# Kernel optimization log

Hardware: AMD Instinct MI355X
Metric: run time of the kernel (lower is better)

The kernel has to match this reference:

```python
import jax, jax.numpy as jnp
import numpy as np

HIDDEN = 512
HEADS = 8
HEAD_DIM = HIDDEN // HEADS
N = 262144
G = 1024
LN_EPS = 1e-5
EPS = 1e-8


def setup_inputs() -> dict:
    key = jax.random.key(0)
    ks = jax.random.split(key, 4)
    x = jax.random.normal(ks[0], (N, HIDDEN), dtype=jnp.float32)
    batch = jnp.sort(jax.random.randint(ks[1], (N,), 0, G, dtype=jnp.int32))
    gamma = jnp.ones((HIDDEN,), jnp.float32)
    beta = jnp.zeros((HIDDEN,), jnp.float32)
    W1 = jax.random.normal(ks[2], (HIDDEN, HIDDEN // 2), dtype=jnp.float32) * (HIDDEN ** -0.5)
    b1 = jnp.zeros((HIDDEN // 2,), jnp.float32)
    W2 = jax.random.normal(ks[3], (HIDDEN // 2, HEADS), dtype=jnp.float32) * ((HIDDEN // 2) ** -0.5)
    b2 = jnp.zeros((HEADS,), jnp.float32)
    return {"x": x, "batch": batch, "gamma": gamma, "beta": beta,
            "W1": W1, "b1": b1, "W2": W2, "b2": b2, "num_graphs": G}


def reference(x, batch, gamma, beta, W1, b1, W2, b2, num_graphs):
    n = x.shape[0]
    # LayerNorm over feature dim
    mu = jnp.mean(x, axis=-1, keepdims=True)
    var = jnp.mean(jnp.square(x - mu), axis=-1, keepdims=True)
    x_norm = (x - mu) * jax.lax.rsqrt(var + LN_EPS) * gamma + beta
    # attention MLP -> per-head logits [N, HEADS]
    h = jax.nn.silu(x_norm @ W1 + b1)
    logits = h @ W2 + b2
    # segment softmax per head (all heads vectorized)
    seg_max = jax.ops.segment_max(logits, batch, num_segments=num_graphs)  # [G, HEADS]
    seg_max = jnp.where(jnp.isfinite(seg_max), seg_max, 0.0)  # guard empty segments
    ex = jnp.exp(logits - seg_max[batch])
    denom = jax.ops.segment_sum(ex, batch, num_segments=num_graphs)  # [G, HEADS]
    denom = jnp.where(denom > 0, denom, 1.0)
    weights = ex / denom[batch]  # [N, HEADS]
    # entropy regularizer
    entropy = -jnp.sum(weights * jnp.log(weights + EPS), axis=0) / num_graphs
    mean_entropy = jnp.mean(entropy)
    # per-head weighted features, flattened back, scatter-sum per graph
    x_split = x.reshape(n, HEADS, HEAD_DIM)
    x_weighted = (x_split * weights[:, :, None]).reshape(n, HIDDEN)
    graph_z = jax.ops.segment_sum(x_weighted, batch, num_segments=num_graphs)  # [G, HIDDEN]
    return graph_z, weights, mean_entropy
```

## Files before the change

kernel.cpp:

```cpp
#include <hip/hip_runtime.h>

#define N_ROWS 262144
#define HID 512
#define HHALF 256
#define HEADS 8
#define GNUM 1024
#define LN_EPS 1e-5f

typedef __bf16 bf16x8 __attribute__((ext_vector_type(8)));
typedef float f32x4 __attribute__((ext_vector_type(4)));

__global__ void k_prep(const float* __restrict__ W1, __bf16* __restrict__ w1t,
                       float* __restrict__ ent) {
    int tid = blockIdx.x * 256 + threadIdx.x;
    if (tid == 0) *ent = 0.f;
    if (tid < HID * HHALF) {
        int n = tid >> 9;
        int k = tid & 511;
        w1t[n * HID + k] = (__bf16)W1[k * HHALF + n];
    }
}

__global__ void k_seg(const int* __restrict__ batch, int* __restrict__ seg) {
    int g = blockIdx.x * 256 + threadIdx.x;
    if (g > GNUM) return;
    int lo = 0, hi = N_ROWS;
    while (lo < hi) {
        int mid = (lo + hi) >> 1;
        if (batch[mid] < g) lo = mid + 1; else hi = mid;
    }
    seg[g] = lo;
}

__global__ __launch_bounds__(256) void k_stats(const float* __restrict__ x,
                                               float2* __restrict__ stats) {
    int wid = threadIdx.x >> 6, lane = threadIdx.x & 63;
    int row = blockIdx.x * 4 + wid;
    const float* xr = x + (size_t)row * HID + lane * 8;
    float4 a = *(const float4*)xr;
    float4 b = *(const float4*)(xr + 4);
    float s = a.x + a.y + a.z + a.w + b.x + b.y + b.z + b.w;
    float q = a.x*a.x + a.y*a.y + a.z*a.z + a.w*a.w
            + b.x*b.x + b.y*b.y + b.z*b.z + b.w*b.w;
    #pragma unroll
    for (int m = 1; m < 64; m <<= 1) {
        s += __shfl_xor(s, m);
        q += __shfl_xor(q, m);
    }
    if (lane == 0) {
        float mu = s * (1.f / HID);
        float var = q * (1.f / HID) - mu * mu;
        stats[row] = make_float2(mu, rsqrtf(var + LN_EPS));
    }
}

__device__ inline bf16x8 make_af(const float* xp, const float* gp, const float* bp,
                                 float rstd, float nmr) {
    float4 xa = *(const float4*)xp;
    float4 xb = *(const float4*)(xp + 4);
    float4 ga = *(const float4*)gp;
    float4 gb = *(const float4*)(gp + 4);
    float4 ba = *(const float4*)bp;
    float4 bb = *(const float4*)(bp + 4);
    float xs[8] = {xa.x, xa.y, xa.z, xa.w, xb.x, xb.y, xb.z, xb.w};
    float gs[8] = {ga.x, ga.y, ga.z, ga.w, gb.x, gb.y, gb.z, gb.w};
    float bs[8] = {ba.x, ba.y, ba.z, ba.w, bb.x, bb.y, bb.z, bb.w};
    bf16x8 r;
    #pragma unroll
    for (int j = 0; j < 8; ++j)
        r[j] = (__bf16)fmaf(fmaf(xs[j], rstd, nmr), gs[j], bs[j]);
    return r;
}

__global__ __launch_bounds__(256) void k_gemm(
    const float* __restrict__ x, const float2* __restrict__ stats,
    const float* __restrict__ gamma, const float* __restrict__ beta,
    const __bf16* __restrict__ w1t, const float* __restrict__ b1,
    const float* __restrict__ W2, const float* __restrict__ b2,
    float* __restrict__ logits)
{
    __shared__ __align__(16) __bf16 ldsb[256 * 72];
    const int tid = threadIdx.x;
    const int wid = tid >> 6, lane = tid & 63;
    const int q = lane >> 4, c = lane & 15;
    const int rowbase = blockIdx.x * 64 + wid * 16;

    f32x4 acc[16];
    #pragma unroll
    for (int t = 0; t < 16; ++t) acc[t] = (f32x4)0.f;

    const int arow = rowbase + c;
    float2 st = stats[arow];
    const float rstd = st.y;
    const float nmr = -st.x * st.y;
    const float* xrow = x + (size_t)arow * HID;

    const int nrow = tid >> 3, seg = tid & 7;

    for (int s8 = 0; s8 < 8; ++s8) {
        const int k0 = s8 * 64;
        __syncthreads();
        #pragma unroll
        for (int it = 0; it < 8; ++it) {
            int n = nrow + it * 32;
            *(uint4*)(ldsb + n * 72 + seg * 8) =
                *(const uint4*)(w1t + n * HID + k0 + seg * 8);
        }
        __syncthreads();

        bf16x8 af0 = make_af(xrow + k0 + q * 8, gamma + k0 + q * 8, beta + k0 + q * 8,
                             rstd, nmr);
        bf16x8 af1 = make_af(xrow + k0 + 32 + q * 8, gamma + k0 + 32 + q * 8,
                             beta + k0 + 32 + q * 8, rstd, nmr);
        #pragma unroll
        for (int t = 0; t < 16; ++t) {
            int n = t * 16 + c;
            bf16x8 bf0 = *(const bf16x8*)(ldsb + n * 72 + q * 8);
            bf16x8 bf1 = *(const bf16x8*)(ldsb + n * 72 + 32 + q * 8);
            acc[t] = __builtin_amdgcn_mfma_f32_16x16x32_bf16(af0, bf0, acc[t], 0, 0, 0);
            acc[t] = __builtin_amdgcn_mfma_f32_16x16x32_bf16(af1, bf1, acc[t], 0, 0, 0);
        }
    }

    float lp[4][8];
    #pragma unroll
    for (int r = 0; r < 4; ++r)
        #pragma unroll
        for (int hd = 0; hd < 8; ++hd) lp[r][hd] = 0.f;

    #pragma unroll
    for (int t = 0; t < 16; ++t) {
        int n = t * 16 + c;
        float b1v = b1[n];
        float4 w2a = *(const float4*)(W2 + n * 8);
        float4 w2b = *(const float4*)(W2 + n * 8 + 4);
        #pragma unroll
        for (int r = 0; r < 4; ++r) {
            float v = acc[t][r] + b1v;
            float h = v / (1.f + __expf(-v));
            lp[r][0] = fmaf(h, w2a.x, lp[r][0]);
            lp[r][1] = fmaf(h, w2a.y, lp[r][1]);
            lp[r][2] = fmaf(h, w2a.z, lp[r][2]);
            lp[r][3] = fmaf(h, w2a.w, lp[r][3]);
            lp[r][4] = fmaf(h, w2b.x, lp[r][4]);
            lp[r][5] = fmaf(h, w2b.y, lp[r][5]);
            lp[r][6] = fmaf(h, w2b.z, lp[r][6]);
            lp[r][7] = fmaf(h, w2b.w, lp[r][7]);
        }
    }
    #pragma unroll
    for (int m = 1; m < 16; m <<= 1)
        #pragma unroll
        for (int r = 0; r < 4; ++r)
            #pragma unroll
            for (int hd = 0; hd < 8; ++hd)
                lp[r][hd] += __shfl_xor(lp[r][hd], m);

    if (c == 0) {
        float4 b2a = *(const float4*)b2;
        float4 b2b = *(const float4*)(b2 + 4);
        #pragma unroll
        for (int r = 0; r < 4; ++r) {
            int orow = rowbase + q * 4 + r;
            float4 o0 = {lp[r][0] + b2a.x, lp[r][1] + b2a.y,
                         lp[r][2] + b2a.z, lp[r][3] + b2a.w};
            float4 o1 = {lp[r][4] + b2b.x, lp[r][5] + b2b.y,
                         lp[r][6] + b2b.z, lp[r][7] + b2b.w};
            *(float4*)(logits + (size_t)orow * 8) = o0;
            *(float4*)(logits + (size_t)orow * 8 + 4) = o1;
        }
    }
}

__global__ __launch_bounds__(256) void k_pool(
    const float* __restrict__ x, const float* __restrict__ logits,
    const int* __restrict__ seg, float* __restrict__ graph_z,
    float* __restrict__ weights, float* __restrict__ ent)
{
    const int g = blockIdx.x;
    const int tid = threadIdx.x;
    const int s = seg[g], e = seg[g + 1];
    const int nrows = e - s;
    __shared__ float smax[8], sinv[8];
    __shared__ float red[4][8];
    __shared__ __align__(16) float wbuf[32][8];

    float acc0 = 0.f, acc1 = 0.f;
    float entl = 0.f;

    if (nrows > 0) {
        const int wid = tid >> 6, lane = tid & 63;
        float mx[8];
        #pragma unroll
        for (int h = 0; h < 8; ++h) mx[h] = -1e30f;
        for (int i = s + tid; i < e; i += 256) {
            float4 l0 = *(const float4*)(logits + (size_t)i * 8);
            float4 l1 = *(const float4*)(logits + (size_t)i * 8 + 4);
            mx[0] = fmaxf(mx[0], l0.x); mx[1] = fmaxf(mx[1], l0.y);
            mx[2] = fmaxf(mx[2], l0.z); mx[3] = fmaxf(mx[3], l0.w);
            mx[4] = fmaxf(mx[4], l1.x); mx[5] = fmaxf(mx[5], l1.y);
            mx[6] = fmaxf(mx[6], l1.z); mx[7] = fmaxf(mx[7], l1.w);
        }
        #pragma unroll
        for (int m = 1; m < 64; m <<= 1)
            #pragma unroll
            for (int h = 0; h < 8; ++h) mx[h] = fmaxf(mx[h], __shfl_xor(mx[h], m));
        if (lane == 0) {
            #pragma unroll
            for (int h = 0; h < 8; ++h) red[wid][h] = mx[h];
        }
        __syncthreads();
        if (tid < 8)
            smax[tid] = fmaxf(fmaxf(red[0][tid], red[1][tid]),
                              fmaxf(red[2][tid], red[3][tid]));
        __syncthreads();
        float sm[8];
        #pragma unroll
        for (int h = 0; h < 8; ++h) sm[h] = smax[h];
        float su[8] = {0, 0, 0, 0, 0, 0, 0, 0};
        for (int i = s + tid; i < e; i += 256) {
            float4 l0 = *(const float4*)(logits + (size_t)i * 8);
            float4 l1 = *(const float4*)(logits + (size_t)i * 8 + 4);
            su[0] += __expf(l0.x - sm[0]); su[1] += __expf(l0.y - sm[1]);
            su[2] += __expf(l0.z - sm[2]); su[3] += __expf(l0.w - sm[3]);
            su[4] += __expf(l1.x - sm[4]); su[5] += __expf(l1.y - sm[5]);
            su[6] += __expf(l1.z - sm[6]); su[7] += __expf(l1.w - sm[7]);
        }
        #pragma unroll
        for (int m = 1; m < 64; m <<= 1)
            #pragma unroll
            for (int h = 0; h < 8; ++h) su[h] += __shfl_xor(su[h], m);
        if (lane == 0) {
            #pragma unroll
            for (int h = 0; h < 8; ++h) red[wid][h] = su[h];
        }
        __syncthreads();
        if (tid < 8) {
            float d = red[0][tid] + red[1][tid] + red[2][tid] + red[3][tid];
            sinv[tid] = 1.f / (d > 0.f ? d : 1.f);
        }
        __syncthreads();
        const int r = tid >> 3, h = tid & 7;
        const float smh = smax[h], ivh = sinv[h];
        const int h0 = tid >> 6, h1 = 4 + (tid >> 6);
        for (int base = 0; base < nrows; base += 32) {
            if (base + r < nrows) {
                int i = s + base + r;
                float w = __expf(logits[(size_t)i * 8 + h] - smh) * ivh;
                wbuf[r][h] = w;
                weights[(size_t)i * 8 + h] = w;
                entl += w * __logf(w + 1e-8f);
            }
            __syncthreads();
            int lim = min(32, nrows - base);
            for (int r2 = 0; r2 < lim; ++r2) {
                const float* xp = x + (size_t)(s + base + r2) * HID;
                acc0 = fmaf(xp[tid], wbuf[r2][h0], acc0);
                acc1 = fmaf(xp[tid + 256], wbuf[r2][h1], acc1);
            }
            __syncthreads();
        }
    }
    graph_z[(size_t)g * HID + tid] = acc0;
    graph_z[(size_t)g * HID + tid + 256] = acc1;

    #pragma unroll
    for (int m = 1; m < 64; m <<= 1) entl += __shfl_xor(entl, m);
    __syncthreads();
    if ((tid & 63) == 0) red[0][tid >> 6] = entl;
    __syncthreads();
    if (tid == 0) {
        float tot = red[0][0] + red[0][1] + red[0][2] + red[0][3];
        atomicAdd(ent, tot * (-1.f / (GNUM * 8.f)));
    }
}

extern "C" void kernel_launch(void* const* d_in, const int* in_sizes, int n_in,
                              void* d_out, int out_size, void* d_ws, size_t ws_size,
                              hipStream_t stream)
{
    const float* x     = (const float*)d_in[0];
    const int*   batch = (const int*)d_in[1];
    const float* gamma = (const float*)d_in[2];
    const float* beta  = (const float*)d_in[3];
    const float* W1    = (const float*)d_in[4];
    const float* b1    = (const float*)d_in[5];
    const float* W2    = (const float*)d_in[6];
    const float* b2    = (const float*)d_in[7];

    char* ws = (char*)d_ws;
    float2* stats  = (float2*)ws;
    float*  logits = (float*)(ws + (size_t)2 * 1024 * 1024);
    __bf16* w1t    = (__bf16*)(ws + (size_t)10 * 1024 * 1024);
    int*    seg    = (int*)(ws + (size_t)10 * 1024 * 1024 + 512 * 1024);

    float* out     = (float*)d_out;
    float* graph_z = out;
    float* weights = out + (size_t)GNUM * HID;
    float* ent     = out + (size_t)GNUM * HID + (size_t)N_ROWS * HEADS;

    k_prep <<<512, 256, 0, stream>>>(W1, w1t, ent);
    k_seg  <<<5, 256, 0, stream>>>(batch, seg);
    k_stats<<<N_ROWS / 4, 256, 0, stream>>>(x, stats);
    k_gemm <<<N_ROWS / 64, 256, 0, stream>>>(x, stats, gamma, beta, w1t, b1, W2, b2, logits);
    k_pool <<<GNUM, 256, 0, stream>>>(x, logits, seg, graph_z, weights, ent);
}
```

Measured before the change: 1.051 ms.

## Fuse LayerNorm stats into GEMM and split pooling into row-tiled atomic kernel

Removes the separate LayerNorm stats kernel by computing row mean and rstd inside the GEMM block, and stages normalized A tiles in LDS so each wave computes a 64-column slice instead of recomputing A per wave. The per-graph pooling kernel is split into a per-graph max and sum kernel plus a row-tiled weighted-pooling kernel over 256-row tiles. That kernel accumulates runs of equal graph ids and flushes them to graph_z with atomics, fixing load imbalance from variable segment sizes. It adds a zeroing kernel and relies on float atomics, so summation order becomes nondeterministic.

```diff
diff --git a/kernel.cpp b/kernel.cpp
--- a/kernel.cpp
+++ b/kernel.cpp
@@ -10,15 +10,17 @@
 typedef __bf16 bf16x8 __attribute__((ext_vector_type(8)));
 typedef float f32x4 __attribute__((ext_vector_type(4)));
 
-__global__ void k_prep(const float* __restrict__ W1, __bf16* __restrict__ w1t,
-                       float* __restrict__ ent) {
+__global__ void k_zero(float4* __restrict__ gz, float* __restrict__ ent) {
+    int t = blockIdx.x * 256 + threadIdx.x;
+    gz[t] = make_float4(0.f, 0.f, 0.f, 0.f);
+    if (t == 0) *ent = 0.f;
+}
+
+__global__ void k_prep(const float* __restrict__ W1, __bf16* __restrict__ w1t) {
     int tid = blockIdx.x * 256 + threadIdx.x;
-    if (tid == 0) *ent = 0.f;
-    if (tid < HID * HHALF) {
-        int n = tid >> 9;
-        int k = tid & 511;
-        w1t[n * HID + k] = (__bf16)W1[k * HHALF + n];
-    }
+    int n = tid >> 9;
+    int k = tid & 511;
+    w1t[n * HID + k] = (__bf16)W1[k * HHALF + n];
 }
 
 __global__ void k_seg(const int* __restrict__ batch, int* __restrict__ seg) {
@@ -32,247 +34,290 @@
     seg[g] = lo;
 }
 
-__global__ __launch_bounds__(256) void k_stats(const float* __restrict__ x,
-                                               float2* __restrict__ stats) {
-    int wid = threadIdx.x >> 6, lane = threadIdx.x & 63;
-    int row = blockIdx.x * 4 + wid;
-    const float* xr = x + (size_t)row * HID + lane * 8;
-    float4 a = *(const float4*)xr;
-    float4 b = *(const float4*)(xr + 4);
-    float s = a.x + a.y + a.z + a.w + b.x + b.y + b.z + b.w;
-    float q = a.x*a.x + a.y*a.y + a.z*a.z + a.w*a.w
-            + b.x*b.x + b.y*b.y + b.z*b.z + b.w*b.w;
-    #pragma unroll
-    for (int m = 1; m < 64; m <<= 1) {
-        s += __shfl_xor(s, m);
-        q += __shfl_xor(q, m);
-    }
-    if (lane == 0) {
-        float mu = s * (1.f / HID);
-        float var = q * (1.f / HID) - mu * mu;
-        stats[row] = make_float2(mu, rsqrtf(var + LN_EPS));
-    }
-}
-
-__device__ inline bf16x8 make_af(const float* xp, const float* gp, const float* bp,
-                                 float rstd, float nmr) {
-    float4 xa = *(const float4*)xp;
-    float4 xb = *(const float4*)(xp + 4);
-    float4 ga = *(const float4*)gp;
-    float4 gb = *(const float4*)(gp + 4);
-    float4 ba = *(const float4*)bp;
-    float4 bb = *(const float4*)(bp + 4);
-    float xs[8] = {xa.x, xa.y, xa.z, xa.w, xb.x, xb.y, xb.z, xb.w};
-    float gs[8] = {ga.x, ga.y, ga.z, ga.w, gb.x, gb.y, gb.z, gb.w};
-    float bs[8] = {ba.x, ba.y, ba.z, ba.w, bb.x, bb.y, bb.z, bb.w};
-    bf16x8 r;
-    #pragma unroll
-    for (int j = 0; j < 8; ++j)
-        r[j] = (__bf16)fmaf(fmaf(xs[j], rstd, nmr), gs[j], bs[j]);
-    return r;
-}
-
 __global__ __launch_bounds__(256) void k_gemm(
-    const float* __restrict__ x, const float2* __restrict__ stats,
-    const float* __restrict__ gamma, const float* __restrict__ beta,
-    const __bf16* __restrict__ w1t, const float* __restrict__ b1,
-    const float* __restrict__ W2, const float* __restrict__ b2,
-    float* __restrict__ logits)
+    const float* __restrict__ x, const float* __restrict__ gamma,
+    const float* __restrict__ beta, const __bf16* __restrict__ w1t,
+    const float* __restrict__ b1, const float* __restrict__ W2,
+    const float* __restrict__ b2, float* __restrict__ logits)
 {
     __shared__ __align__(16) __bf16 ldsb[256 * 72];
+    __shared__ __align__(16) __bf16 ldsa[64 * 72];
+    __shared__ float s_rstd[64], s_nmr[64];
+    __shared__ float s_lp[4][64][8];
+
     const int tid = threadIdx.x;
     const int wid = tid >> 6, lane = tid & 63;
     const int q = lane >> 4, c = lane & 15;
-    const int rowbase = blockIdx.x * 64 + wid * 16;
-
-    f32x4 acc[16];
-    #pragma unroll
-    for (int t = 0; t < 16; ++t) acc[t] = (f32x4)0.f;
-
-    const int arow = rowbase + c;
-    float2 st = stats[arow];
-    const float rstd = st.y;
-    const float nmr = -st.x * st.y;
-    const float* xrow = x + (size_t)arow * HID;
-
-    const int nrow = tid >> 3, seg = tid & 7;
-
-    for (int s8 = 0; s8 < 8; ++s8) {
-        const int k0 = s8 * 64;
+    const int rowbase = blockIdx.x * 64;
+    const float* xt = x + (size_t)rowbase * HID;
+    const int r4 = tid >> 2, qt = tid & 3;
+
+    {
+        const float4* xp = (const float4*)(xt + r4 * HID + qt * 128);
+        float s = 0.f, qq = 0.f;
+        #pragma unroll 8
+        for (int i = 0; i < 32; ++i) {
+            float4 v = xp[i];
+            s += v.x + v.y + v.z + v.w;
+            qq = fmaf(v.x, v.x, fmaf(v.y, v.y, fmaf(v.z, v.z, fmaf(v.w, v.w, qq))));
+        }
+        s += __shfl_xor(s, 1); qq += __shfl_xor(qq, 1);
+        s += __shfl_xor(s, 2); qq += __shfl_xor(qq, 2);
+        if (qt == 0) {
+            float mu = s * (1.f / HID);
+            float var = qq * (1.f / HID) - mu * mu;
+            float rs = rsqrtf(var + LN_EPS);
+            s_rstd[r4] = rs; s_nmr[r4] = -mu * rs;
+        }
+    }
+
+    f32x4 acc[4][4];
+    #pragma unroll
+    for (int a = 0; a < 4; ++a)
+        #pragma unroll
+        for (int b = 0; b < 4; ++b) acc[a][b] = (f32x4)0.f;
+
+    const int nrow = tid >> 3, segt = tid & 7;
+    const int colbase = wid * 64;
+
+    for (int ch = 0; ch < 8; ++ch) {
+        const int k0 = ch * 64;
         __syncthreads();
         #pragma unroll
         for (int it = 0; it < 8; ++it) {
             int n = nrow + it * 32;
-            *(uint4*)(ldsb + n * 72 + seg * 8) =
-                *(const uint4*)(w1t + n * HID + k0 + seg * 8);
+            *(uint4*)(ldsb + n * 72 + segt * 8) =
+                *(const uint4*)(w1t + n * HID + k0 + segt * 8);
+        }
+        {
+            float rs = s_rstd[r4], nm = s_nmr[r4];
+            const float4* xp = (const float4*)(xt + r4 * HID + k0 + qt * 16);
+            const float4* gp = (const float4*)(gamma + k0 + qt * 16);
+            const float4* bp = (const float4*)(beta + k0 + qt * 16);
+            #pragma unroll
+            for (int j = 0; j < 2; ++j) {
+                float4 xa = xp[2 * j], xb = xp[2 * j + 1];
+                float4 ga = gp[2 * j], gb = gp[2 * j + 1];
+                float4 ba = bp[2 * j], bb = bp[2 * j + 1];
+                bf16x8 o;
+                o[0] = (__bf16)fmaf(fmaf(xa.x, rs, nm), ga.x, ba.x);
+                o[1] = (__bf16)fmaf(fmaf(xa.y, rs, nm), ga.y, ba.y);
+                o[2] = (__bf16)fmaf(fmaf(xa.z, rs, nm), ga.z, ba.z);
+                o[3] = (__bf16)fmaf(fmaf(xa.w, rs, nm), ga.w, ba.w);
+                o[4] = (__bf16)fmaf(fmaf(xb.x, rs, nm), gb.x, bb.x);
+                o[5] = (__bf16)fmaf(fmaf(xb.y, rs, nm), gb.y, bb.y);
+                o[6] = (__bf16)fmaf(fmaf(xb.z, rs, nm), gb.z, bb.z);
+                o[7] = (__bf16)fmaf(fmaf(xb.w, rs, nm), gb.w, bb.w);
+                *(bf16x8*)(ldsa + r4 * 72 + qt * 16 + j * 8) = o;
+            }
         }
         __syncthreads();
-
-        bf16x8 af0 = make_af(xrow + k0 + q * 8, gamma + k0 + q * 8, beta + k0 + q * 8,
-                             rstd, nmr);
-        bf16x8 af1 = make_af(xrow + k0 + 32 + q * 8, gamma + k0 + 32 + q * 8,
-                             beta + k0 + 32 + q * 8, rstd, nmr);
-        #pragma unroll
-        for (int t = 0; t < 16; ++t) {
-            int n = t * 16 + c;
-            bf16x8 bf0 = *(const bf16x8*)(ldsb + n * 72 + q * 8);
-            bf16x8 bf1 = *(const bf16x8*)(ldsb + n * 72 + 32 + q * 8);
-            acc[t] = __builtin_amdgcn_mfma_f32_16x16x32_bf16(af0, bf0, acc[t], 0, 0, 0);
-            acc[t] = __builtin_amdgcn_mfma_f32_16x16x32_bf16(af1, bf1, acc[t], 0, 0, 0);
-        }
-    }
-
-    float lp[4][8];
-    #pragma unroll
-    for (int r = 0; r < 4; ++r)
-        #pragma unroll
-        for (int hd = 0; hd < 8; ++hd) lp[r][hd] = 0.f;
-
-    #pragma unroll
-    for (int t = 0; t < 16; ++t) {
-        int n = t * 16 + c;
-        float b1v = b1[n];
-        float4 w2a = *(const float4*)(W2 + n * 8);
-        float4 w2b = *(const float4*)(W2 + n * 8 + 4);
-        #pragma unroll
-        for (int r = 0; r < 4; ++r) {
-            float v = acc[t][r] + b1v;
-            float h = v / (1.f + __expf(-v));
-            lp[r][0] = fmaf(h, w2a.x, lp[r][0]);
-            lp[r][1] = fmaf(h, w2a.y, lp[r][1]);
-            lp[r][2] = fmaf(h, w2a.z, lp[r][2]);
-            lp[r][3] = fmaf(h, w2a.w, lp[r][3]);
-            lp[r][4] = fmaf(h, w2b.x, lp[r][4]);
-            lp[r][5] = fmaf(h, w2b.y, lp[r][5]);
-            lp[r][6] = fmaf(h, w2b.z, lp[r][6]);
-            lp[r][7] = fmaf(h, w2b.w, lp[r][7]);
-        }
-    }
-    #pragma unroll
-    for (int m = 1; m < 16; m <<= 1)
+        bf16x8 bfr[4][2];
+        #pragma unroll
+        for (int cg = 0; cg < 4; ++cg) {
+            int n = colbase + cg * 16 + c;
+            bfr[cg][0] = *(const bf16x8*)(ldsb + n * 72 + q * 8);
+            bfr[cg][1] = *(const bf16x8*)(ldsb + n * 72 + 32 + q * 8);
+        }
+        #pragma unroll
+        for (int rg = 0; rg < 4; ++rg) {
+            int m = rg * 16 + c;
+            bf16x8 a0 = *(const bf16x8*)(ldsa + m * 72 + q * 8);
+            bf16x8 a1 = *(const bf16x8*)(ldsa + m * 72 + 32 + q * 8);
+            #pragma unroll
+            for (int cg = 0; cg < 4; ++cg) {
+                acc[rg][cg] = __builtin_amdgcn_mfma_f32_16x16x32_bf16(a0, bfr[cg][0], acc[rg][cg], 0, 0, 0);
+                acc[rg][cg] = __builtin_amdgcn_mfma_f32_16x16x32_bf16(a1, bfr[cg][1], acc[rg][cg], 0, 0, 0);
+            }
+        }
+    }
+
+    #pragma unroll
+    for (int rg = 0; rg < 4; ++rg) {
+        float lp[4][8];
         #pragma unroll
         for (int r = 0; r < 4; ++r)
             #pragma unroll
-            for (int hd = 0; hd < 8; ++hd)
-                lp[r][hd] += __shfl_xor(lp[r][hd], m);
-
-    if (c == 0) {
-        float4 b2a = *(const float4*)b2;
-        float4 b2b = *(const float4*)(b2 + 4);
-        #pragma unroll
-        for (int r = 0; r < 4; ++r) {
-            int orow = rowbase + q * 4 + r;
-            float4 o0 = {lp[r][0] + b2a.x, lp[r][1] + b2a.y,
-                         lp[r][2] + b2a.z, lp[r][3] + b2a.w};
-            float4 o1 = {lp[r][4] + b2b.x, lp[r][5] + b2b.y,
-                         lp[r][6] + b2b.z, lp[r][7] + b2b.w};
-            *(float4*)(logits + (size_t)orow * 8) = o0;
-            *(float4*)(logits + (size_t)orow * 8 + 4) = o1;
-        }
-    }
-}
-
-__global__ __launch_bounds__(256) void k_pool(
+            for (int hd = 0; hd < 8; ++hd) lp[r][hd] = 0.f;
+        #pragma unroll
+        for (int cg = 0; cg < 4; ++cg) {
+            int n = colbase + cg * 16 + c;
+            float b1v = b1[n];
+            float4 w2a = *(const float4*)(W2 + n * 8);
+            float4 w2b = *(const float4*)(W2 + n * 8 + 4);
+            #pragma unroll
+            for (int r = 0; r < 4; ++r) {
+                float v = acc[rg][cg][r] + b1v;
+                float h = v / (1.f + __expf(-v));
+                lp[r][0] = fmaf(h, w2a.x, lp[r][0]);
+                lp[r][1] = fmaf(h, w2a.y, lp[r][1]);
+                lp[r][2] = fmaf(h, w2a.z, lp[r][2]);
+                lp[r][3] = fmaf(h, w2a.w, lp[r][3]);
+                lp[r][4] = fmaf(h, w2b.x, lp[r][4]);
+                lp[r][5] = fmaf(h, w2b.y, lp[r][5]);
+                lp[r][6] = fmaf(h, w2b.z, lp[r][6]);
+                lp[r][7] = fmaf(h, w2b.w, lp[r][7]);
+            }
+        }
+        #pragma unroll
+        for (int m = 1; m < 16; m <<= 1)
+            #pragma unroll
+            for (int r = 0; r < 4; ++r)
+                #pragma unroll
+                for (int hd = 0; hd < 8; ++hd)
+                    lp[r][hd] += __shfl_xor(lp[r][hd], m);
+        if (c == 0) {
+            #pragma unroll
+            for (int r = 0; r < 4; ++r)
+                #pragma unroll
+                for (int hd = 0; hd < 8; ++hd)
+                    s_lp[wid][rg * 16 + q * 4 + r][hd] = lp[r][hd];
+        }
+    }
+    __syncthreads();
+    #pragma unroll
+    for (int idx = tid; idx < 512; idx += 256) {
+        int row = idx >> 3, hd = idx & 7;
+        float v = s_lp[0][row][hd] + s_lp[1][row][hd] + s_lp[2][row][hd]
+                + s_lp[3][row][hd] + b2[hd];
+        logits[(size_t)(rowbase + row) * 8 + hd] = v;
+    }
+}
+
+__global__ __launch_bounds__(256) void k_gmax(
+    const float* __restrict__ logits, const int* __restrict__ seg,
+    float* __restrict__ smax8, float* __restrict__ sinv8)
+{
+    const int g = blockIdx.x, tid = threadIdx.x;
+    const int s = seg[g], e = seg[g + 1];
+    const int wid = tid >> 6, lane = tid & 63;
+    __shared__ float red[4][8];
+    __shared__ float smax[8];
+
+    float mx[8];
+    #pragma unroll
+    for (int h = 0; h < 8; ++h) mx[h] = -1e30f;
+    for (int i = s + tid; i < e; i += 256) {
+        float4 l0 = *(const float4*)(logits + (size_t)i * 8);
+        float4 l1 = *(const float4*)(logits + (size_t)i * 8 + 4);
+        mx[0] = fmaxf(mx[0], l0.x); mx[1] = fmaxf(mx[1], l0.y);
+        mx[2] = fmaxf(mx[2], l0.z); mx[3] = fmaxf(mx[3], l0.w);
+        mx[4] = fmaxf(mx[4], l1.x); mx[5] = fmaxf(mx[5], l1.y);
+        mx[6] = fmaxf(mx[6], l1.z); mx[7] = fmaxf(mx[7], l1.w);
+    }
+    #pragma unroll
+    for (int m = 1; m < 64; m <<= 1)
+        #pragma unroll
+        for (int h = 0; h < 8; ++h) mx[h] = fmaxf(mx[h], __shfl_xor(mx[h], m));
+    if (lane == 0) {
+        #pragma unroll
+        for (int h = 0; h < 8; ++h) red[wid][h] = mx[h];
+    }
+    __syncthreads();
+    if (tid < 8)
+        smax[tid] = fmaxf(fmaxf(red[0][tid], red[1][tid]),
+                          fmaxf(red[2][tid], red[3][tid]));
+    __syncthreads();
+    float sm[8];
+    #pragma unroll
+    for (int h = 0; h < 8; ++h) sm[h] = smax[h];
+    float su[8] = {0, 0, 0, 0, 0, 0, 0, 0};
+    for (int i = s + tid; i < e; i += 256) {
+        float4 l0 = *(const float4*)(logits + (size_t)i * 8);
+        float4 l1 = *(const float4*)(logits + (size_t)i * 8 + 4);
+        su[0] += __expf(l0.x - sm[0]); su[1] += __expf(l0.y - sm[1]);
+        su[2] += __expf(l0.z - sm[2]); su[3] += __expf(l0.w - sm[3]);
+        su[4] += __expf(l1.x - sm[4]); su[5] += __expf(l1.y - sm[5]);
+        su[6] += __expf(l1.z - sm[6]); su[7] += __expf(l1.w - sm[7]);
+    }
+    #pragma unroll
+    for (int m = 1; m < 64; m <<= 1)
+        #pragma unroll
+        for (int h = 0; h < 8; ++h) su[h] += __shfl_xor(su[h], m);
+    __syncthreads();
+    if (lane == 0) {
+        #pragma unroll
+        for (int h = 0; h < 8; ++h) red[wid][h] = su[h];
+    }
+    __syncthreads();
+    if (tid < 8) {
+        float d = red[0][tid] + red[1][tid] + red[2][tid] + red[3][tid];
+        float sv = smax[tid];
+        if (e == s) sv = 0.f;
+        if (!(d > 0.f)) d = 1.f;
+        smax8[g * 8 + tid] = sv;
+        sinv8[g * 8 + tid] = 1.f / d;
+    }
+}
+
+__global__ __launch_bounds__(256) void k_wpool(
     const float* __restrict__ x, const float* __restrict__ logits,
-    const int* __restrict__ seg, float* __restrict__ graph_z,
+    const int* __restrict__ batch, const float* __restrict__ smax8,
+    const float* __restrict__ sinv8, float* __restrict__ graph_z,
     float* __restrict__ weights, float* __restrict__ ent)
 {
-    const int g = blockIdx.x;
+    __shared__ float wsm[256][8];
+    __shared__ int sbatch[256];
+    __shared__ float red[4];
+
     const int tid = threadIdx.x;
-    const int s = seg[g], e = seg[g + 1];
-    const int nrows = e - s;
-    __shared__ float smax[8], sinv[8];
-    __shared__ float red[4][8];
-    __shared__ __align__(16) float wbuf[32][8];
-
-    float acc0 = 0.f, acc1 = 0.f;
+    const int wid = tid >> 6, lane = tid & 63;
+    const int base = blockIdx.x * 256;
+    const int i = base + tid;
+
+    const int g = batch[i];
+    sbatch[tid] = g;
+    float4 l0 = *(const float4*)(logits + (size_t)i * 8);
+    float4 l1 = *(const float4*)(logits + (size_t)i * 8 + 4);
+    float w[8];
+    {
+        const float* smp = smax8 + g * 8;
+        const float* ivp = sinv8 + g * 8;
+        w[0] = __expf(l0.x - smp[0]) * ivp[0];
+        w[1] = __expf(l0.y - smp[1]) * ivp[1];
+        w[2] = __expf(l0.z - smp[2]) * ivp[2];
+        w[3] = __expf(l0.w - smp[3]) * ivp[3];
+        w[4] = __expf(l1.x - smp[4]) * ivp[4];
+        w[5] = __expf(l1.y - smp[5]) * ivp[5];
+        w[6] = __expf(l1.z - smp[6]) * ivp[6];
+        w[7] = __expf(l1.w - smp[7]) * ivp[7];
+    }
     float entl = 0.f;
-
-    if (nrows > 0) {
-        const int wid = tid >> 6, lane = tid & 63;
-        float mx[8];
-        #pragma unroll
-        for (int h = 0; h < 8; ++h) mx[h] = -1e30f;
-        for (int i = s + tid; i < e; i += 256) {
-            float4 l0 = *(const float4*)(logits + (size_t)i * 8);
-            float4 l1 = *(const float4*)(logits + (size_t)i * 8 + 4);
-            mx[0] = fmaxf(mx[0], l0.x); mx[1] = fmaxf(mx[1], l0.y);
-            mx[2] = fmaxf(mx[2], l0.z); mx[3] = fmaxf(mx[3], l0.w);
-            mx[4] = fmaxf(mx[4], l1.x); mx[5] = fmaxf(mx[5], l1.y);
-            mx[6] = fmaxf(mx[6], l1.z); mx[7] = fmaxf(mx[7], l1.w);
-        }
-        #pragma unroll
-        for (int m = 1; m < 64; m <<= 1)
-            #pragma unroll
-            for (int h = 0; h < 8; ++h) mx[h] = fmaxf(mx[h], __shfl_xor(mx[h], m));
-        if (lane == 0) {
-            #pragma unroll
-            for (int h = 0; h < 8; ++h) red[wid][h] = mx[h];
-        }
-        __syncthreads();
-        if (tid < 8)
-            smax[tid] = fmaxf(fmaxf(red[0][tid], red[1][tid]),
-                              fmaxf(red[2][tid], red[3][tid]));
-        __syncthreads();
-        float sm[8];
-        #pragma unroll
-        for (int h = 0; h < 8; ++h) sm[h] = smax[h];
-        float su[8] = {0, 0, 0, 0, 0, 0, 0, 0};
-        for (int i = s + tid; i < e; i += 256) {
-            float4 l0 = *(const float4*)(logits + (size_t)i * 8);
-            float4 l1 = *(const float4*)(logits + (size_t)i * 8 + 4);
-            su[0] += __expf(l0.x - sm[0]); su[1] += __expf(l0.y - sm[1]);
-            su[2] += __expf(l0.z - sm[2]); su[3] += __expf(l0.w - sm[3]);
-            su[4] += __expf(l1.x - sm[4]); su[5] += __expf(l1.y - sm[5]);
-            su[6] += __expf(l1.z - sm[6]); su[7] += __expf(l1.w - sm[7]);
-        }
-        #pragma unroll
-        for (int m = 1; m < 64; m <<= 1)
-            #pragma unroll
-            for (int h = 0; h < 8; ++h) su[h] += __shfl_xor(su[h], m);
-        if (lane == 0) {
-            #pragma unroll
-            for (int h = 0; h < 8; ++h) red[wid][h] = su[h];
-        }
-        __syncthreads();
-        if (tid < 8) {
-            float d = red[0][tid] + red[1][tid] + red[2][tid] + red[3][tid];
-            sinv[tid] = 1.f / (d > 0.f ? d : 1.f);
-        }
-        __syncthreads();
-        const int r = tid >> 3, h = tid & 7;
-        const float smh = smax[h], ivh = sinv[h];
-        const int h0 = tid >> 6, h1 = 4 + (tid >> 6);
-        for (int base = 0; base < nrows; base += 32) {
-            if (base + r < nrows) {
-                int i = s + base + r;
-                float w = __expf(logits[(size_t)i * 8 + h] - smh) * ivh;
-                wbuf[r][h] = w;
-                weights[(size_t)i * 8 + h] = w;
-                entl += w * __logf(w + 1e-8f);
-            }
-            __syncthreads();
-            int lim = min(32, nrows - base);
-            for (int r2 = 0; r2 < lim; ++r2) {
-                const float* xp = x + (size_t)(s + base + r2) * HID;
-                acc0 = fmaf(xp[tid], wbuf[r2][h0], acc0);
-                acc1 = fmaf(xp[tid + 256], wbuf[r2][h1], acc1);
-            }
-            __syncthreads();
-        }
-    }
-    graph_z[(size_t)g * HID + tid] = acc0;
-    graph_z[(size_t)g * HID + tid + 256] = acc1;
+    #pragma unroll
+    for (int h = 0; h < 8; ++h) {
+        entl = fmaf(w[h], __logf(w[h] + 1e-8f), entl);
+        wsm[tid][h] = w[h];
+    }
+    *(float4*)(weights + (size_t)i * 8)     = make_float4(w[0], w[1], w[2], w[3]);
+    *(float4*)(weights + (size_t)i * 8 + 4) = make_float4(w[4], w[5], w[6], w[7]);
 
     #pragma unroll
     for (int m = 1; m < 64; m <<= 1) entl += __shfl_xor(entl, m);
-    __syncthreads();
-    if ((tid & 63) == 0) red[0][tid >> 6] = entl;
-    __syncthreads();
-    if (tid == 0) {
-        float tot = red[0][0] + red[0][1] + red[0][2] + red[0][3];
-        atomicAdd(ent, tot * (-1.f / (GNUM * 8.f)));
-    }
+    if (lane == 0) red[wid] = entl;
+    __syncthreads();
+    if (tid == 0)
+        atomicAdd(ent, (red[0] + red[1] + red[2] + red[3]) * (-1.f / (GNUM * 8.f)));
+
+    const int col = tid * 2;
+    const int h = tid >> 5;
+    const float* xb = x + (size_t)base * HID + col;
+    float ax = 0.f, ay = 0.f;
+    int curg = sbatch[0];
+    #pragma unroll 4
+    for (int r2 = 0; r2 < 256; ++r2) {
+        int g2 = sbatch[r2];
+        if (g2 != curg) {
+            atomicAdd(&graph_z[(size_t)curg * HID + col], ax);
+            atomicAdd(&graph_z[(size_t)curg * HID + col + 1], ay);
+            ax = 0.f; ay = 0.f; curg = g2;
+        }
+        float wv = wsm[r2][h];
+        float2 xv = *(const float2*)(xb + (size_t)r2 * HID);
+        ax = fmaf(wv, xv.x, ax);
+        ay = fmaf(wv, xv.y, ay);
+    }
+    atomicAdd(&graph_z[(size_t)curg * HID + col], ax);
+    atomicAdd(&graph_z[(size_t)curg * HID + col + 1], ay);
 }
 
 extern "C" void kernel_launch(void* const* d_in, const int* in_sizes, int n_in,
@@ -289,19 +334,21 @@
     const float* b2    = (const float*)d_in[7];
 
     char* ws = (char*)d_ws;
-    float2* stats  = (float2*)ws;
-    float*  logits = (float*)(ws + (size_t)2 * 1024 * 1024);
-    __bf16* w1t    = (__bf16*)(ws + (size_t)10 * 1024 * 1024);
-    int*    seg    = (int*)(ws + (size_t)10 * 1024 * 1024 + 512 * 1024);
+    float*  logits = (float*)ws;
+    __bf16* w1t    = (__bf16*)(ws + (size_t)8 * 1024 * 1024);
+    int*    seg    = (int*)(ws + (size_t)8 * 1024 * 1024 + 512 * 1024);
+    float*  smax8  = (float*)(ws + (size_t)9 * 1024 * 1024);
+    float*  sinv8  = (float*)(ws + (size_t)9 * 1024 * 1024 + 64 * 1024);
 
     float* out     = (float*)d_out;
     float* graph_z = out;
     float* weights = out + (size_t)GNUM * HID;
     float* ent     = out + (size_t)GNUM * HID + (size_t)N_ROWS * HEADS;
 
-    k_prep <<<512, 256, 0, stream>>>(W1, w1t, ent);
+    k_zero <<<512, 256, 0, stream>>>((float4*)graph_z, ent);
+    k_prep <<<512, 256, 0, stream>>>(W1, w1t);
     k_seg  <<<5, 256, 0, stream>>>(batch, seg);
-    k_stats<<<N_ROWS / 4, 256, 0, stream>>>(x, stats);
-    k_gemm <<<N_ROWS / 64, 256, 0, stream>>>(x, stats, gamma, beta, w1t, b1, W2, b2, logits);
-    k_pool <<<GNUM, 256, 0, stream>>>(x, logits, seg, graph_z, weights, ent);
-}
+    k_gemm <<<N_ROWS / 64, 256, 0, stream>>>(x, gamma, beta, w1t, b1, W2, b2, logits);
+    k_gmax <<<GNUM, 256, 0, stream>>>(logits, seg, smax8, sinv8);
+    k_wpool<<<GNUM, 256, 0, stream>>>(x, logits, batch, smax8, sinv8, graph_z, weights, ent);
+}
```

Result: slower. 1.073 ms (+2.0%).
